# Performance work log

Hardware: AMD Instinct MI355X
Metric: run time of the kernel (lower is better)

The kernel has to match this reference:

```python
import jax, jax.numpy as jnp
import numpy as np

B, S, H = 2, 2048, 2048
N_HEADS = 16
HEAD_DIM = H // N_HEADS  # 128


def apply_rotary(x, cos, sin):
    # x: (B, n_heads, S, head_dim); cos/sin: (S, head_dim//2)
    d = x.shape[-1] // 2
    x1, x2 = x[..., :d], x[..., d:]
    c = cos[None, None, :x.shape[2]]
    s = sin[None, None, :x.shape[2]]
    return jnp.concatenate([x1 * c - x2 * s, x2 * c + x1 * s], axis=-1)


def setup_inputs() -> dict:
    key = jax.random.key(0)
    k1, k2, k3 = jax.random.split(key, 3)
    x = jax.random.normal(k1, (B, S, H), dtype=jnp.float32)
    qkv_w = jax.random.normal(k2, (3 * H, H), dtype=jnp.float32) * (1.0 / np.sqrt(H))
    o_w = jax.random.normal(k3, (H, H), dtype=jnp.float32) * (1.0 / np.sqrt(H))
    # rotary tables, half head_dim
    inv_freq = 1.0 / (10000.0 ** (jnp.arange(0, HEAD_DIM // 2, dtype=jnp.float32) / (HEAD_DIM // 2)))
    t = jnp.arange(S, dtype=jnp.float32)
    freqs = jnp.outer(t, inv_freq)  # (S, head_dim//2)
    cos, sin = jnp.cos(freqs), jnp.sin(freqs)
    # True = masked (strictly upper triangular)
    causal_mask = jnp.triu(jnp.ones((S, S), dtype=bool), k=1)
    return {"x": x, "qkv_w": qkv_w, "o_w": o_w, "cos": cos, "sin": sin,
            "causal_mask": causal_mask}


def reference(x, qkv_w, o_w, cos, sin, causal_mask):
    Bx, Sx, Hx = x.shape
    qkv = jnp.einsum('bsh,oh->bso', x, qkv_w)  # (B,S,3H)
    qkv = qkv.reshape(Bx, Sx, 3, N_HEADS, HEAD_DIM)
    q, k, v = qkv[:, :, 0], qkv[:, :, 1], qkv[:, :, 2]
    q = jnp.transpose(q, (0, 2, 1, 3))  # (B,nh,S,hd)
    k = jnp.transpose(k, (0, 2, 1, 3))
    v = jnp.transpose(v, (0, 2, 1, 3))
    q = apply_rotary(q, cos, sin)
    k = apply_rotary(k, cos, sin)
    scale = 1.0 / jnp.sqrt(jnp.asarray(HEAD_DIM, dtype=x.dtype))
    attn = jnp.einsum('bnqd,bnkd->bnqk', q, k) * scale
    attn = jnp.where(causal_mask[None, None], -jnp.inf, attn)
    attn = jax.nn.softmax(attn, axis=-1)
    out = jnp.einsum('bnqk,bnkd->bnqd', attn, v)
    out = jnp.transpose(out, (0, 2, 1, 3)).reshape(Bx, Sx, Hx)
    return jnp.einsum('bsh,oh->bso', out, o_w)
```

## Files before the change

kernel.cpp:

```cpp
#include <hip/hip_runtime.h>
#include <hip/hip_bf16.h>
#include <stdint.h>

typedef __attribute__((ext_vector_type(4))) float f32x4;
typedef __attribute__((ext_vector_type(8))) short s16x8;
typedef __attribute__((ext_vector_type(4))) short s16x4;

#define SWZ(g, row) ((((g) & ~7) | (((g) ^ ((row) & 7)) & 7)))

__device__ __forceinline__ unsigned short f2bf(float f) {
  unsigned u = __builtin_bit_cast(unsigned, f);
  u += 0x7fffu + ((u >> 16) & 1u);
  return (unsigned short)(u >> 16);
}

__device__ __forceinline__ void gld16(const void* g, void* l) {
  __builtin_amdgcn_global_load_lds(
      (const __attribute__((address_space(1))) void*)g,
      (__attribute__((address_space(3))) void*)l, 16, 0, 0);
}

__global__ void cvt_f32_to_bf16(const float* __restrict__ src,
                                unsigned short* __restrict__ dst, int n4) {
  int i = blockIdx.x * blockDim.x + threadIdx.x;
  if (i >= n4) return;
  float4 v = ((const float4*)src)[i];
  s16x4 o;
  o[0] = (short)f2bf(v.x); o[1] = (short)f2bf(v.y);
  o[2] = (short)f2bf(v.z); o[3] = (short)f2bf(v.w);
  ((s16x4*)dst)[i] = o;
}

#define STAGE384(BB, KT) \
  { char* dA = smem + (BB) * 65536; \
    char* dB = dA + 16384; \
    _Pragma("unroll") for (int rr = 0; rr < 2; ++rr) { \
      const int G = rr * 512 + tid; const int row = G >> 3, g = G & 7; \
      gld16((const char*)(Aorg + (size_t)row * 2048 + (size_t)(KT) * 64) + (SWZ(g, row) << 4), \
            dA + rr * 8192 + tid * 16); } \
    _Pragma("unroll") for (int rr = 0; rr < 6; ++rr) { \
      const int G = rr * 512 + tid; const int row = G >> 3, g = G & 7; \
      gld16((const char*)(Borg + (size_t)row * 2048 + (size_t)(KT) * 64) + (SWZ(g, row) << 4), \
            dB + rr * 8192 + tid * 16); } }

#define CPH384(KS) \
  { s16x8 av[4], bv[6]; \
    _Pragma("unroll") for (int j = 0; j < 4; ++j) { \
      const int ra = wm * 64 + j * 16 + lg; \
      av[j] = *(const s16x8*)(sA + ra * 128 + (SWZ(4 * (KS) + hg, ra) << 4)); } \
    _Pragma("unroll") for (int b = 0; b < 6; ++b) { \
      const int cb = (b >> 1) * 128 + wn * 16 + (b & 1) * 64 + lg; \
      bv[b] = *(const s16x8*)(sB + cb * 128 + (SWZ(4 * (KS) + hg, cb) << 4)); } \
    _Pragma("unroll") for (int j = 0; j < 4; ++j) \
      _Pragma("unroll") for (int b = 0; b < 6; ++b) \
        acc[j][b] = __builtin_amdgcn_mfma_f32_16x16x32_bf16(av[j], bv[b], acc[j][b], 0, 0, 0); }

__global__ __launch_bounds__(512, 1) void gemm_qkv_384(
    const unsigned short* __restrict__ A,
    const unsigned short* __restrict__ Bt,
    const float* __restrict__ cosT, const float* __restrict__ sinT,
    unsigned short* __restrict__ qOut, unsigned short* __restrict__ kOut,
    unsigned short* __restrict__ vtOut)
{
  __shared__ char smem[131072];
  const int tid = (int)threadIdx.x;
  const int wid = tid >> 6, l = tid & 63;
  const int lg = l & 15, hg = l >> 4;
  const int wm = wid >> 2, wn = wid & 3;
  const int s = ((int)blockIdx.x & 7) * 64 + ((int)blockIdx.x >> 3);
  const int bm0 = (s & 31) * 128, bn0 = (s >> 5) * 384;

  const unsigned short* Aorg = A + (size_t)bm0 * 2048;
  const unsigned short* Borg = Bt + (size_t)bn0 * 2048;

  f32x4 acc[4][6] = {};

  STAGE384(0, 0)
  for (int t = 0; t < 31; ++t) {
    STAGE384((t & 1) ^ 1, t + 1)
    asm volatile("s_waitcnt vmcnt(8)" ::: "memory");
    __builtin_amdgcn_s_barrier();
    asm volatile("" ::: "memory");
    const char* sA = smem + (t & 1) * 65536;
    const char* sB = sA + 16384;
    __builtin_amdgcn_s_setprio(1);
    CPH384(0)
    CPH384(1)
    __builtin_amdgcn_s_setprio(0);
    asm volatile("" ::: "memory");
    __builtin_amdgcn_s_barrier();
    asm volatile("" ::: "memory");
  }
  {
    asm volatile("s_waitcnt vmcnt(0)" ::: "memory");
    __builtin_amdgcn_s_barrier();
    asm volatile("" ::: "memory");
    const char* sA = smem + 65536;
    const char* sB = sA + 16384;
    CPH384(0)
    CPH384(1)
  }

  #pragma unroll
  for (int j = 0; j < 4; ++j) {
    const int grow0 = bm0 + wm * 64 + j * 16 + hg * 4;
    const int b_ = grow0 >> 11;
    #pragma unroll
    for (int cg = 0; cg < 3; ++cg) {
      const int og = (bn0 >> 7) + cg;
      const int tt = og >> 4, h = og & 15;
      const int d = wn * 16 + lg;
      if (tt < 2) {
        unsigned short* dst = (tt == 0) ? qOut : kOut;
        #pragma unroll
        for (int r = 0; r < 4; ++r) {
          const int gr = grow0 + r;
          const int s1 = gr & 2047;
          const float x1 = acc[j][cg * 2 + 0][r];
          const float x2 = acc[j][cg * 2 + 1][r];
          const float cv = cosT[s1 * 64 + d];
          const float sv = sinT[s1 * 64 + d];
          const size_t base = (((size_t)b_ * 16 + h) * 2048 + s1) * 128;
          dst[base + d]      = f2bf(x1 * cv - x2 * sv);
          dst[base + d + 64] = f2bf(x2 * cv + x1 * sv);
        }
      } else {
        const int s0 = grow0 & 2047;
        s16x4 p1, p2;
        #pragma unroll
        for (int r = 0; r < 4; ++r) {
          p1[r] = (short)f2bf(acc[j][cg * 2 + 0][r]);
          p2[r] = (short)f2bf(acc[j][cg * 2 + 1][r]);
        }
        *(s16x4*)(vtOut + (((size_t)b_ * 16 + h) * 128 + d)      * 2048 + s0) = p1;
        *(s16x4*)(vtOut + (((size_t)b_ * 16 + h) * 128 + d + 64) * 2048 + s0) = p2;
      }
    }
  }
}

template<int EPI>
__global__ __launch_bounds__(256) void gemm_bt(
    const unsigned short* __restrict__ A,
    const unsigned short* __restrict__ Bt,
    float* __restrict__ C, int N, int K)
{
  __shared__ char smem[32768];
  const int tid = (int)threadIdx.x;
  const int w  = tid >> 6, l = tid & 63;
  const int lg = l & 15, hg = l >> 4;
  const int bn0 = (int)blockIdx.x * 128, bm0 = (int)blockIdx.y * 128;

  f32x4 acc[2][8] = {};
  const int nkt = K >> 6;
  for (int kt = 0; kt < nkt; ++kt) {
    __syncthreads();
    for (int i = 0; i < 4; ++i) {
      const int G = w * 256 + i * 64 + l;
      const int row = G >> 3, g = G & 7;
      const int gs = SWZ(g, row);
      gld16((const char*)(A  + (size_t)(bm0 + row) * K + (size_t)kt * 64) + (gs << 4),
            smem + w * 4096 + i * 1024);
      gld16((const char*)(Bt + (size_t)(bn0 + row) * K + (size_t)kt * 64) + (gs << 4),
            smem + 16384 + w * 4096 + i * 1024);
    }
    asm volatile("s_waitcnt vmcnt(0)" ::: "memory");
    __syncthreads();
    for (int ks = 0; ks < 2; ++ks) {
      s16x8 af[2], bfr[8];
      for (int ai = 0; ai < 2; ++ai) {
        const int ra = w * 32 + ai * 16 + lg;
        const int gr = SWZ(4 * ks + hg, ra);
        af[ai] = *(const s16x8*)(smem + ra * 128 + (gr << 4));
      }
      for (int bi = 0; bi < 8; ++bi) {
        const int rb = bi * 16 + lg;
        const int gr = SWZ(4 * ks + hg, rb);
        bfr[bi] = *(const s16x8*)(smem + 16384 + rb * 128 + (gr << 4));
      }
      for (int ai = 0; ai < 2; ++ai)
        for (int bi = 0; bi < 8; ++bi)
          acc[ai][bi] = __builtin_amdgcn_mfma_f32_16x16x32_bf16(
              af[ai], bfr[bi], acc[ai][bi], 0, 0, 0);
    }
  }

  for (int ai = 0; ai < 2; ++ai)
    for (int bi = 0; bi < 8; ++bi) {
      const int col  = bn0 + bi * 16 + lg;
      const int row0 = bm0 + w * 32 + ai * 16 + hg * 4;
      for (int r = 0; r < 4; ++r)
        C[(size_t)(row0 + r) * N + col] = acc[ai][bi][r];
    }
}

__global__ __launch_bounds__(256) void attn_fwd(
    const unsigned short* __restrict__ Qp, const unsigned short* __restrict__ Kp,
    const unsigned short* __restrict__ Vt, unsigned short* __restrict__ AO)
{
  __shared__ char sK[16384];
  __shared__ char sV[16384];
  __shared__ char sP[8192];

  const int tid = (int)threadIdx.x, w = tid >> 6, l = tid & 63;
  const int lg = l & 15, hg = l >> 4;
  const int bid = (int)blockIdx.x;
  const int p = bid >> 8, c = bid & 255;
  const int j = c >> 5, bh = c & 31;
  const int qt = (p == 0) ? j : (p == 1) ? 31 - j : (p == 2) ? 8 + j : 23 - j;
  const size_t qkBase = (size_t)bh * 2048 * 128;
  const int qw0 = qt * 64 + w * 16;
  const int qi = qw0 + lg;

  s16x8 qf[4];
  for (int ks = 0; ks < 4; ++ks)
    qf[ks] = *(const s16x8*)(Qp + qkBase + (size_t)(qw0 + lg) * 128 + ks * 32 + hg * 8);

  f32x4 acc_o[8] = {};
  float mrun = -1e30f, lrun = 0.f;
  const float SCALE = 0.08838834764831845f;
  const float L2E = 1.4426950408889634f;
  const float CS = SCALE * L2E;

  const int nkv = qt + 1;
  for (int kv = 0; kv < nkv; ++kv) {
    const int kv0 = kv * 64;
    __syncthreads();
    for (int i = 0; i < 4; ++i) {
      const int G = w * 256 + i * 64 + l;
      const int rk = G >> 4, gk = G & 15;
      gld16((const char*)(Kp + qkBase + (size_t)(kv0 + rk) * 128) + (SWZ(gk, rk) << 4),
            sK + w * 4096 + i * 1024);
      const int rv = G >> 3, gv = G & 7;
      gld16((const char*)(Vt + qkBase + (size_t)rv * 2048 + kv0) + (SWZ(gv, rv) << 4),
            sV + w * 4096 + i * 1024);
    }
    asm volatile("s_waitcnt vmcnt(0)" ::: "memory");
    __syncthreads();

    f32x4 accs[4] = {};
    for (int ks = 0; ks < 4; ++ks)
      for (int kf = 0; kf < 4; ++kf) {
        const int row = kf * 16 + lg;
        const int g = SWZ(4 * ks + hg, row);
        s16x8 kfrag = *(const s16x8*)(sK + row * 256 + (g << 4));
        accs[kf] = __builtin_amdgcn_mfma_f32_16x16x32_bf16(kfrag, qf[ks], accs[kf], 0, 0, 0);
      }

    const bool diag = (kv == qt);
    float raw[4][4];
    float mt = -1e30f;
    #pragma unroll
    for (int kf = 0; kf < 4; ++kf)
      #pragma unroll
      for (int r = 0; r < 4; ++r) {
        float s = accs[kf][r];
        if (diag) {
          const int jj = kv0 + kf * 16 + hg * 4 + r;
          s = (jj > qi) ? -1e30f : s;
        }
        raw[kf][r] = s;
        mt = fmaxf(mt, s);
      }
    mt = fmaxf(mt, __shfl_xor(mt, 16));
    mt = fmaxf(mt, __shfl_xor(mt, 32));
    mt *= SCALE;
    if (!__all(mt - mrun <= 8.0f)) {
      const float mnew = fmaxf(mrun, mt);
      const float alpha = exp2f((mrun - mnew) * L2E);
      float ar[4];
      #pragma unroll
      for (int r = 0; r < 4; ++r) ar[r] = __shfl(alpha, hg * 4 + r);
      #pragma unroll
      for (int f = 0; f < 8; ++f)
        #pragma unroll
        for (int r = 0; r < 4; ++r) acc_o[f][r] *= ar[r];
      lrun *= alpha;
      mrun = mnew;
    }
    const float mL = mrun * L2E;
    float ls = 0.f;
    char* pw = sP + w * 2048;
    #pragma unroll
    for (int kf = 0; kf < 4; ++kf) {
      s16x4 pk;
      #pragma unroll
      for (int r = 0; r < 4; ++r) {
        const float e = exp2f(raw[kf][r] * CS - mL);
        ls += e;
        pk[r] = (short)f2bf(e);
      }
      const int j0 = kf * 16 + hg * 4;
      *(s16x4*)(pw + lg * 128 + (SWZ(j0 >> 3, lg) << 4) + ((j0 * 2) & 15)) = pk;
    }
    ls += __shfl_xor(ls, 16);
    ls += __shfl_xor(ls, 32);
    lrun += ls;
    asm volatile("" ::: "memory");

    for (int jc = 0; jc < 2; ++jc) {
      const int gp = SWZ(hg + 4 * jc, lg);
      s16x8 pa = *(const s16x8*)(pw + lg * 128 + (gp << 4));
      for (int f = 0; f < 8; ++f) {
        const int rv = f * 16 + lg;
        const int gv = SWZ(hg + 4 * jc, rv);
        s16x8 vb = *(const s16x8*)(sV + rv * 128 + (gv << 4));
        acc_o[f] = __builtin_amdgcn_mfma_f32_16x16x32_bf16(pa, vb, acc_o[f], 0, 0, 0);
      }
    }
  }

  float linv[4];
  for (int r = 0; r < 4; ++r) linv[r] = 1.0f / __shfl(lrun, hg * 4 + r);
  const int b = bh >> 4, h = bh & 15;
  for (int f = 0; f < 8; ++f) {
    const int d = h * 128 + f * 16 + lg;
    for (int r = 0; r < 4; ++r) {
      const int srow = qw0 + hg * 4 + r;
      AO[((size_t)(b * 2048 + srow)) * 2048 + d] = f2bf(acc_o[f][r] * linv[r]);
    }
  }
}

extern "C" void kernel_launch(void* const* d_in, const int* in_sizes, int n_in,
                              void* d_out, int out_size, void* d_ws, size_t ws_size,
                              hipStream_t stream) {
  const float* x    = (const float*)d_in[0];
  const float* qkvw = (const float*)d_in[1];
  const float* ow   = (const float*)d_in[2];
  const float* cosT = (const float*)d_in[3];
  const float* sinT = (const float*)d_in[4];
  float* out = (float*)d_out;

  unsigned short* X16  = (unsigned short*)d_ws;
  unsigned short* W16  = X16  + (size_t)8388608;
  unsigned short* OW16 = W16  + (size_t)12582912;
  unsigned short* Qp   = OW16 + (size_t)4194304;
  unsigned short* Kp   = Qp   + (size_t)8388608;
  unsigned short* Vtp  = Kp   + (size_t)8388608;
  unsigned short* AO   = Vtp  + (size_t)8388608;

  cvt_f32_to_bf16<<<8192, 256, 0, stream>>>(x, X16, 2097152);
  cvt_f32_to_bf16<<<12288, 256, 0, stream>>>(qkvw, W16, 3145728);
  cvt_f32_to_bf16<<<4096, 256, 0, stream>>>(ow, OW16, 1048576);

  gemm_qkv_384<<<512, 512, 0, stream>>>(X16, W16, cosT, sinT, Qp, Kp, Vtp);

  attn_fwd<<<1024, 256, 0, stream>>>(Qp, Kp, Vtp, AO);

  dim3 g2(16, 32);
  gemm_bt<0><<<g2, 256, 0, stream>>>(AO, OW16, out, 2048, 2048);
}
```

Baseline: 251.6 us.

## Stagger k-halves across warp rows in QKV GEMM and rewrite output projection GEMM

In the QKV GEMM, the two warp rows now process the two k-substeps in opposite order. Each loads both fragment sets from LDS up front and overlaps the second barrier with the MFMAs, rather than running compute-then-barrier serially. The output projection GEMM is replaced by a new 256-wide-tile, 512-thread kernel. It uses double-buffered direct-to-LDS loads, the same staggered schedule and a swizzled block order for L2 locality. The cost is higher register use from holding two fragment sets at once, and the output GEMM now launches only 256 blocks.

```diff
diff --git a/kernel.cpp b/kernel.cpp
--- a/kernel.cpp
+++ b/kernel.cpp
@@ -43,17 +43,18 @@
       gld16((const char*)(Borg + (size_t)row * 2048 + (size_t)(KT) * 64) + (SWZ(g, row) << 4), \
             dB + rr * 8192 + tid * 16); } }
 
-#define CPH384(KS) \
-  { s16x8 av[4], bv[6]; \
-    _Pragma("unroll") for (int j = 0; j < 4; ++j) { \
-      const int ra = wm * 64 + j * 16 + lg; \
-      av[j] = *(const s16x8*)(sA + ra * 128 + (SWZ(4 * (KS) + hg, ra) << 4)); } \
-    _Pragma("unroll") for (int b = 0; b < 6; ++b) { \
-      const int cb = (b >> 1) * 128 + wn * 16 + (b & 1) * 64 + lg; \
-      bv[b] = *(const s16x8*)(sB + cb * 128 + (SWZ(4 * (KS) + hg, cb) << 4)); } \
-    _Pragma("unroll") for (int j = 0; j < 4; ++j) \
-      _Pragma("unroll") for (int b = 0; b < 6; ++b) \
-        acc[j][b] = __builtin_amdgcn_mfma_f32_16x16x32_bf16(av[j], bv[b], acc[j][b], 0, 0, 0); }
+#define RD384(AV, BV, KS) \
+  _Pragma("unroll") for (int j = 0; j < 4; ++j) { \
+    const int ra = wm * 64 + j * 16 + lg; \
+    AV[j] = *(const s16x8*)(sA + ra * 128 + (SWZ(4 * (KS) + hg, ra) << 4)); } \
+  _Pragma("unroll") for (int b = 0; b < 6; ++b) { \
+    const int cb = (b >> 1) * 128 + wn * 16 + (b & 1) * 64 + lg; \
+    BV[b] = *(const s16x8*)(sB + cb * 128 + (SWZ(4 * (KS) + hg, cb) << 4)); }
+
+#define MM384(AV, BV) \
+  _Pragma("unroll") for (int j = 0; j < 4; ++j) \
+    _Pragma("unroll") for (int b = 0; b < 6; ++b) \
+      acc[j][b] = __builtin_amdgcn_mfma_f32_16x16x32_bf16(AV[j], BV[b], acc[j][b], 0, 0, 0);
 
 __global__ __launch_bounds__(512, 1) void gemm_qkv_384(
     const unsigned short* __restrict__ A,
@@ -80,25 +81,32 @@
     STAGE384((t & 1) ^ 1, t + 1)
     asm volatile("s_waitcnt vmcnt(8)" ::: "memory");
     __builtin_amdgcn_s_barrier();
-    asm volatile("" ::: "memory");
     const char* sA = smem + (t & 1) * 65536;
     const char* sB = sA + 16384;
+    const int ksA = wm, ksB = 1 - wm;
+    s16x8 avA[4], bvA[6], avB[4], bvB[6];
+    RD384(avA, bvA, ksA)
+    RD384(avB, bvB, ksB)
     __builtin_amdgcn_s_setprio(1);
-    CPH384(0)
-    CPH384(1)
+    MM384(avA, bvA)
     __builtin_amdgcn_s_setprio(0);
-    asm volatile("" ::: "memory");
-    __builtin_amdgcn_s_barrier();
-    asm volatile("" ::: "memory");
+    asm volatile("s_waitcnt lgkmcnt(0)" ::: "memory");
+    __builtin_amdgcn_s_barrier();
+    __builtin_amdgcn_sched_barrier(0);
+    __builtin_amdgcn_s_setprio(1);
+    MM384(avB, bvB)
+    __builtin_amdgcn_s_setprio(0);
   }
   {
     asm volatile("s_waitcnt vmcnt(0)" ::: "memory");
     __builtin_amdgcn_s_barrier();
-    asm volatile("" ::: "memory");
     const char* sA = smem + 65536;
     const char* sB = sA + 16384;
-    CPH384(0)
-    CPH384(1)
+    s16x8 avA[4], bvA[6], avB[4], bvB[6];
+    RD384(avA, bvA, 0)
+    RD384(avB, bvB, 1)
+    MM384(avA, bvA)
+    MM384(avB, bvB)
   }
 
   #pragma unroll
@@ -139,59 +147,93 @@
   }
 }
 
-template<int EPI>
-__global__ __launch_bounds__(256) void gemm_bt(
+#define STAGEOP(BB, KT) \
+  { char* dA = smem + (BB) * 49152; \
+    char* dB = dA + 16384; \
+    _Pragma("unroll") for (int rr = 0; rr < 2; ++rr) { \
+      const int G = rr * 512 + tid; const int row = G >> 3, g = G & 7; \
+      gld16((const char*)(Aorg + (size_t)row * 2048 + (size_t)(KT) * 64) + (SWZ(g, row) << 4), \
+            dA + rr * 8192 + tid * 16); } \
+    _Pragma("unroll") for (int rr = 0; rr < 4; ++rr) { \
+      const int G = rr * 512 + tid; const int row = G >> 3, g = G & 7; \
+      gld16((const char*)(Borg + (size_t)row * 2048 + (size_t)(KT) * 64) + (SWZ(g, row) << 4), \
+            dB + rr * 8192 + tid * 16); } }
+
+#define RDOP(AV, BV, KS) \
+  _Pragma("unroll") for (int j = 0; j < 4; ++j) { \
+    const int ra = wm * 64 + j * 16 + lg; \
+    AV[j] = *(const s16x8*)(sA + ra * 128 + (SWZ(4 * (KS) + hg, ra) << 4)); } \
+  _Pragma("unroll") for (int b = 0; b < 4; ++b) { \
+    const int cb = b * 64 + wn * 16 + lg; \
+    BV[b] = *(const s16x8*)(sB + cb * 128 + (SWZ(4 * (KS) + hg, cb) << 4)); }
+
+#define MMOP(AV, BV) \
+  _Pragma("unroll") for (int j = 0; j < 4; ++j) \
+    _Pragma("unroll") for (int b = 0; b < 4; ++b) \
+      acc[j][b] = __builtin_amdgcn_mfma_f32_16x16x32_bf16(AV[j], BV[b], acc[j][b], 0, 0, 0);
+
+__global__ __launch_bounds__(512, 1) void gemm_op_256(
     const unsigned short* __restrict__ A,
     const unsigned short* __restrict__ Bt,
-    float* __restrict__ C, int N, int K)
+    float* __restrict__ C)
 {
-  __shared__ char smem[32768];
+  __shared__ char smem[98304];
   const int tid = (int)threadIdx.x;
-  const int w  = tid >> 6, l = tid & 63;
+  const int wid = tid >> 6, l = tid & 63;
   const int lg = l & 15, hg = l >> 4;
-  const int bn0 = (int)blockIdx.x * 128, bm0 = (int)blockIdx.y * 128;
-
-  f32x4 acc[2][8] = {};
-  const int nkt = K >> 6;
-  for (int kt = 0; kt < nkt; ++kt) {
-    __syncthreads();
-    for (int i = 0; i < 4; ++i) {
-      const int G = w * 256 + i * 64 + l;
-      const int row = G >> 3, g = G & 7;
-      const int gs = SWZ(g, row);
-      gld16((const char*)(A  + (size_t)(bm0 + row) * K + (size_t)kt * 64) + (gs << 4),
-            smem + w * 4096 + i * 1024);
-      gld16((const char*)(Bt + (size_t)(bn0 + row) * K + (size_t)kt * 64) + (gs << 4),
-            smem + 16384 + w * 4096 + i * 1024);
-    }
+  const int wm = wid >> 2, wn = wid & 3;
+  const int s = ((int)blockIdx.x & 7) * 32 + ((int)blockIdx.x >> 3);
+  const int bm0 = (s & 31) * 128, bn0 = (s >> 5) * 256;
+
+  const unsigned short* Aorg = A + (size_t)bm0 * 2048;
+  const unsigned short* Borg = Bt + (size_t)bn0 * 2048;
+
+  f32x4 acc[4][4] = {};
+
+  STAGEOP(0, 0)
+  for (int t = 0; t < 31; ++t) {
+    STAGEOP((t & 1) ^ 1, t + 1)
+    asm volatile("s_waitcnt vmcnt(6)" ::: "memory");
+    __builtin_amdgcn_s_barrier();
+    const char* sA = smem + (t & 1) * 49152;
+    const char* sB = sA + 16384;
+    const int ksA = wm, ksB = 1 - wm;
+    s16x8 avA[4], bvA[4], avB[4], bvB[4];
+    RDOP(avA, bvA, ksA)
+    RDOP(avB, bvB, ksB)
+    __builtin_amdgcn_s_setprio(1);
+    MMOP(avA, bvA)
+    __builtin_amdgcn_s_setprio(0);
+    asm volatile("s_waitcnt lgkmcnt(0)" ::: "memory");
+    __builtin_amdgcn_s_barrier();
+    __builtin_amdgcn_sched_barrier(0);
+    __builtin_amdgcn_s_setprio(1);
+    MMOP(avB, bvB)
+    __builtin_amdgcn_s_setprio(0);
+  }
+  {
     asm volatile("s_waitcnt vmcnt(0)" ::: "memory");
-    __syncthreads();
-    for (int ks = 0; ks < 2; ++ks) {
-      s16x8 af[2], bfr[8];
-      for (int ai = 0; ai < 2; ++ai) {
-        const int ra = w * 32 + ai * 16 + lg;
-        const int gr = SWZ(4 * ks + hg, ra);
-        af[ai] = *(const s16x8*)(smem + ra * 128 + (gr << 4));
-      }
-      for (int bi = 0; bi < 8; ++bi) {
-        const int rb = bi * 16 + lg;
-        const int gr = SWZ(4 * ks + hg, rb);
-        bfr[bi] = *(const s16x8*)(smem + 16384 + rb * 128 + (gr << 4));
-      }
-      for (int ai = 0; ai < 2; ++ai)
-        for (int bi = 0; bi < 8; ++bi)
-          acc[ai][bi] = __builtin_amdgcn_mfma_f32_16x16x32_bf16(
-              af[ai], bfr[bi], acc[ai][bi], 0, 0, 0);
-    }
-  }
-
-  for (int ai = 0; ai < 2; ++ai)
-    for (int bi = 0; bi < 8; ++bi) {
-      const int col  = bn0 + bi * 16 + lg;
-      const int row0 = bm0 + w * 32 + ai * 16 + hg * 4;
+    __builtin_amdgcn_s_barrier();
+    const char* sA = smem + 49152;
+    const char* sB = sA + 16384;
+    s16x8 avA[4], bvA[4], avB[4], bvB[4];
+    RDOP(avA, bvA, 0)
+    RDOP(avB, bvB, 1)
+    MMOP(avA, bvA)
+    MMOP(avB, bvB)
+  }
+
+  #pragma unroll
+  for (int j = 0; j < 4; ++j) {
+    const int row0 = bm0 + wm * 64 + j * 16 + hg * 4;
+    #pragma unroll
+    for (int b = 0; b < 4; ++b) {
+      const int col = bn0 + b * 64 + wn * 16 + lg;
+      #pragma unroll
       for (int r = 0; r < 4; ++r)
-        C[(size_t)(row0 + r) * N + col] = acc[ai][bi][r];
-    }
+        C[(size_t)(row0 + r) * 2048 + col] = acc[j][b][r];
+    }
+  }
 }
 
 __global__ __launch_bounds__(256) void attn_fwd(
@@ -348,6 +390,5 @@
 
   attn_fwd<<<1024, 256, 0, stream>>>(Qp, Kp, Vtp, AO);
 
-  dim3 g2(16, 32);
-  gemm_bt<0><<<g2, 256, 0, stream>>>(AO, OW16, out, 2048, 2048);
-}
+  gemm_op_256<<<256, 512, 0, stream>>>(AO, OW16, out);
+}
```

After: 236.4 us. 6.0% less time.
